# Kernel optimization log

Measured on AMD Instinct MI355X. Metric: run time of the kernel, lower is better.

Reference implementation:

```python
import jax, jax.numpy as jnp
import numpy as np

NEG = -1e30  # log-zero surrogate (avoid -inf for stable grads)


def ctc_neg_log_like(log_probs, targets, input_lengths, target_lengths):
    """Standard CTC (blank=0) negative log-likelihood, mean over batch.
    Math-equivalent to k2 topo-compile + intersect_dense + log-semiring tot_scores.
    log_probs: [B,T,C] logits or log-probs (re-normalized, as GradExpNormalize does).
    """
    lp = jax.nn.log_softmax(log_probs, axis=-1)
    B, T, C = lp.shape
    S = targets.shape[1]
    L = 2 * S + 1  # blank-interleaved extended label sequence length
    ext = jnp.zeros((B, L), jnp.int32).at[:, 1::2].set(targets.astype(jnp.int32))
    prev2 = jnp.pad(ext[:, :-2], ((0, 0), (2, 0)), constant_values=-1)
    can_skip = (ext != prev2) & (ext != 0)  # skip transition allowed

    lp_tb = jnp.moveaxis(lp, 1, 0)  # [T,B,C] for scan over time
    start = jnp.full((B, L), NEG, lp.dtype).at[:, 0].set(0.0).at[:, 1].set(0.0)
    alpha0 = start + jnp.take_along_axis(lp_tb[0], ext, axis=1)  # [B,L]

    def step(alpha, xs):
        lp_t, t = xs
        emit_t = jnp.take_along_axis(lp_t, ext, axis=1)  # [B,L]
        s1 = jnp.pad(alpha[:, :-1], ((0, 0), (1, 0)), constant_values=NEG)
        s2 = jnp.where(can_skip,
                       jnp.pad(alpha[:, :-2], ((0, 0), (2, 0)), constant_values=NEG),
                       NEG)
        new = jnp.logaddexp(jnp.logaddexp(alpha, s1), s2) + emit_t
        # freeze alpha once past this utterance's length
        new = jnp.where((t < input_lengths)[:, None], new, alpha)
        return new, None

    ts = jnp.arange(1, T, dtype=jnp.int32)
    alpha, _ = jax.lax.scan(step, alpha0, (lp_tb[1:], ts))

    idx1 = (2 * target_lengths).astype(jnp.int32)
    idx2 = jnp.maximum(2 * target_lengths - 1, 0).astype(jnp.int32)
    a1 = jnp.take_along_axis(alpha, idx1[:, None], axis=1)[:, 0]
    a2 = jnp.take_along_axis(alpha, idx2[:, None], axis=1)[:, 0]
    a2 = jnp.where(target_lengths > 0, a2, NEG)
    tot_scores = jnp.logaddexp(a1, a2)  # per-utterance log-likelihood
    return -jnp.mean(tot_scores)  # reduction='mean'


def setup_inputs() -> dict:
    key = jax.random.key(0)
    k1, k2, k3, k4 = jax.random.split(key, 4)
    B, T, C, S = 64, 2048, 1024, 256
    log_probs = jax.random.normal(k1, (B, T, C), dtype=jnp.float32)
    targets = 1 + jax.random.randint(k2, (B, S), 0, C - 1, dtype=jnp.int32)  # labels in [1, C)
    input_lengths = jax.random.randint(k3, (B,), T // 2, T + 1, dtype=jnp.int32)
    target_lengths = jax.random.randint(k4, (B,), S // 2, S + 1, dtype=jnp.int32)
    return {"log_probs": log_probs, "targets": targets,
            "input_lengths": input_lengths, "target_lengths": target_lengths}


def reference(log_probs, targets, input_lengths, target_lengths):
    return ctc_neg_log_like(log_probs, targets, input_lengths, target_lengths)
```

## Files before the change

kernel.cpp:

```cpp
#include <hip/hip_runtime.h>
#include <hip/hip_fp16.h>
#include <math.h>

typedef __attribute__((ext_vector_type(4))) float f32x4;
typedef __attribute__((ext_vector_type(2))) unsigned int u32x2;

#define SB() __builtin_amdgcn_sched_barrier(0)
#define WAITV(n)                                              \
  do {                                                        \
    asm volatile("s_waitcnt vmcnt(" #n ")" ::: "memory");     \
    SB();                                                     \
  } while (0)
#define LD2(dst, ptr, OFF)                                           \
  asm volatile("global_load_dwordx2 %0, %1, off offset:" OFF         \
               : "=v"(dst) : "v"(ptr) : "memory")
#define LD4(dst, ptr, OFF)                                           \
  asm volatile("global_load_dwordx4 %0, %1, off offset:" OFF         \
               : "=v"(dst) : "v"(ptr) : "memory")

__device__ inline float wave_max64(float v) {
#pragma unroll
  for (int off = 32; off > 0; off >>= 1) v = fmaxf(v, __shfl_xor(v, off, 64));
  return v;
}
__device__ inline float wave_sum64(float v) {
#pragma unroll
  for (int off = 32; off > 0; off >>= 1) v += __shfl_xor(v, off, 64);
  return v;
}
__device__ inline float wave_max_dpp(float x) {
  int xi = __float_as_int(x);
  x = fmaxf(x, __int_as_float(__builtin_amdgcn_update_dpp(xi, xi, 0x111, 0xf, 0xf, false)));
  xi = __float_as_int(x);
  x = fmaxf(x, __int_as_float(__builtin_amdgcn_update_dpp(xi, xi, 0x112, 0xf, 0xf, false)));
  xi = __float_as_int(x);
  x = fmaxf(x, __int_as_float(__builtin_amdgcn_update_dpp(xi, xi, 0x114, 0xf, 0xf, false)));
  xi = __float_as_int(x);
  x = fmaxf(x, __int_as_float(__builtin_amdgcn_update_dpp(xi, xi, 0x118, 0xf, 0xf, false)));
  xi = __float_as_int(x);
  x = fmaxf(x, __int_as_float(__builtin_amdgcn_update_dpp(xi, xi, 0x142, 0xa, 0xf, false)));
  xi = __float_as_int(x);
  x = fmaxf(x, __int_as_float(__builtin_amdgcn_update_dpp(xi, xi, 0x143, 0xc, 0xf, false)));
  return __int_as_float(__builtin_amdgcn_readlane(__float_as_int(x), 63));
}
__device__ inline float lane_shr1(float x) {
  return __int_as_float(__builtin_amdgcn_update_dpp(
      0, __float_as_int(x), 0x138, 0xf, 0xf, true));
}

__device__ __forceinline__ void k1_body(
    const float* __restrict__ lp, const int* __restrict__ targets,
    char* __restrict__ gw, float* __restrict__ qw, int t0, int T, int CB,
    int QS, int S, int b, int tq, float* rowbuf) {
  const int lane = threadIdx.x & 63;
  const int w = threadIdx.x >> 6;
  const int tloc = tq * 4 + w;
  const int t = t0 + tloc;
  if (t >= T) return;
  const int4 tg4 = *(const int4*)(targets + (size_t)b * S + 4 * lane);

  const float* row = lp + ((size_t)b * T + t) * 1024;
  const float4 v0 = *(const float4*)(row + 4 * lane);
  const float4 v1 = *(const float4*)(row + 256 + 4 * lane);
  const float4 v2 = *(const float4*)(row + 512 + 4 * lane);
  const float4 v3 = *(const float4*)(row + 768 + 4 * lane);
  float mx = fmaxf(fmaxf(fmaxf(v0.x, v0.y), fmaxf(v0.z, v0.w)),
                   fmaxf(fmaxf(v1.x, v1.y), fmaxf(v1.z, v1.w)));
  mx = fmaxf(mx, fmaxf(fmaxf(fmaxf(v2.x, v2.y), fmaxf(v2.z, v2.w)),
                       fmaxf(fmaxf(v3.x, v3.y), fmaxf(v3.z, v3.w))));
  mx = wave_max64(mx);
  float sm = __expf(v0.x - mx) + __expf(v0.y - mx) + __expf(v0.z - mx) +
             __expf(v0.w - mx) + __expf(v1.x - mx) + __expf(v1.y - mx) +
             __expf(v1.z - mx) + __expf(v1.w - mx) + __expf(v2.x - mx) +
             __expf(v2.y - mx) + __expf(v2.z - mx) + __expf(v2.w - mx) +
             __expf(v3.x - mx) + __expf(v3.y - mx) + __expf(v3.z - mx) +
             __expf(v3.w - mx);
  sm = wave_sum64(sm);
  const float lse = mx + __logf(sm);
  *(float4*)(rowbuf + 4 * lane) = v0;
  *(float4*)(rowbuf + 256 + 4 * lane) = v1;
  *(float4*)(rowbuf + 512 + 4 * lane) = v2;
  *(float4*)(rowbuf + 768 + 4 * lane) = v3;
  const float e0 = __expf(rowbuf[tg4.x] - lse);
  const float e1 = __expf(rowbuf[tg4.y] - lse);
  const float e2 = __expf(rowbuf[tg4.z] - lse);
  const float e3 = __expf(rowbuf[tg4.w] - lse);
  const unsigned h0 = __half_as_ushort(__float2half(e0));
  const unsigned h1 = __half_as_ushort(__float2half(e1));
  const unsigned h2 = __half_as_ushort(__float2half(e2));
  const unsigned h3 = __half_as_ushort(__float2half(e3));
  char* gr = gw + ((size_t)b * CB + tloc) * 544;
  *(uint2*)(gr + 8 * lane) = make_uint2(h0 | (h1 << 16), h2 | (h3 << 16));
  if (lane == 0) qw[(size_t)b * QS + tloc] = __expf(rowbuf[0] - lse);
}

__global__ __launch_bounds__(256) void k1_std(
    const float* __restrict__ lp, const int* __restrict__ targets,
    char* __restrict__ gw, float* __restrict__ qw, int t0, int T, int CB,
    int QS, int S) {
  __shared__ __align__(16) float rowbuf4[4][1024];
  k1_body(lp, targets, gw, qw, t0, T, CB, QS, S, blockIdx.y, blockIdx.x,
          rowbuf4[threadIdx.x >> 6]);
}

#define DECL8(P)                                                     \
  u32x2 P##v0, P##v1, P##v2, P##v3, P##v4, P##v5, P##v6, P##v7;      \
  f32x4 P##qL, P##qH;

#define ISS8(P)                                                      \
  do {                                                               \
    LD2(P##v0, gpA_, "0");    LD2(P##v1, gpA_, "544");               \
    LD2(P##v2, gpA_, "1088"); LD2(P##v3, gpA_, "1632");              \
    LD2(P##v4, gpB_, "0");    LD2(P##v5, gpB_, "544");               \
    LD2(P##v6, gpB_, "1088"); LD2(P##v7, gpB_, "1632");              \
    LD4(P##qL, gq_, "0");     LD4(P##qH, gq_, "16");                 \
    gpA_ += 4352; gpB_ += 4352; gq_ += 8;                            \
  } while (0)

#define KSR(du, qv)                                                           \
  {                                                                           \
    const float px = __half2float(__ushort_as_half((unsigned short)((du).x))); \
    const float py = __half2float(__ushort_as_half((unsigned short)((du).x >> 16))); \
    const float pz = __half2float(__ushort_as_half((unsigned short)((du).y))); \
    const float pw = __half2float(__ushort_as_half((unsigned short)((du).y >> 16))); \
    const float hm1 = lane_shr1(a7);                                          \
    const float n0 = (a0 + hm1) * (qv);                                       \
    const float n1 = __fmaf_rn(sk1, hm1, a1 + a0) * px;                       \
    const float n2 = (a2 + a1) * (qv);                                        \
    const float n3 = __fmaf_rn(sk3, a1, a3 + a2) * py;                        \
    const float n4 = (a4 + a3) * (qv);                                        \
    const float n5 = __fmaf_rn(sk5, a3, a5 + a4) * pz;                        \
    const float n6 = (a6 + a5) * (qv);                                        \
    const float n7 = __fmaf_rn(sk7, a5, a7 + a6) * pw;                        \
    const float n8 = (a8 + a7) * (qv);                                        \
    a0 = n0; a1 = n1; a2 = n2; a3 = n3; a4 = n4;                              \
    a5 = n5; a6 = n6; a7 = n7; a8 = n8;                                       \
  }

#define RESC()                                                            \
  {                                                                       \
    float m_ = fmaxf(fmaxf(fmaxf(fmaxf(a0, a1), fmaxf(a2, a3)),           \
                           fmaxf(fmaxf(a4, a5), fmaxf(a6, a7))), a8);     \
    m_ = wave_max_dpp(m_);                                                \
    const int e_ =                                                        \
        (m_ > 0.f) ? (int)((__float_as_uint(m_) >> 23) & 255u) - 127 : 0; \
    a0 = ldexpf(a0, -e_); a1 = ldexpf(a1, -e_); a2 = ldexpf(a2, -e_);     \
    a3 = ldexpf(a3, -e_); a4 = ldexpf(a4, -e_); a5 = ldexpf(a5, -e_);     \
    a6 = ldexpf(a6, -e_); a7 = ldexpf(a7, -e_); a8 = ldexpf(a8, -e_);     \
    E += e_;                                                              \
  }

#define COMP8(P, rem)                                            \
  do {                                                           \
    if ((rem) >= 8) {                                            \
      KSR(P##v0, (P##qL).x) KSR(P##v1, (P##qL).y)                \
      KSR(P##v2, (P##qL).z) KSR(P##v3, (P##qL).w)                \
      KSR(P##v4, (P##qH).x) KSR(P##v5, (P##qH).y)                \
      KSR(P##v6, (P##qH).z) KSR(P##v7, (P##qH).w) RESC()         \
    } else {                                                     \
      KSR(P##v0, (P##qL).x)                                      \
      if ((rem) > 1) KSR(P##v1, (P##qL).y)                       \
      if ((rem) > 2) KSR(P##v2, (P##qL).z)                       \
      if ((rem) > 3) KSR(P##v3, (P##qL).w)                       \
      if ((rem) > 4) KSR(P##v4, (P##qH).x)                       \
      if ((rem) > 5) KSR(P##v5, (P##qH).y)                       \
      if ((rem) > 6) KSR(P##v6, (P##qH).z)                       \
      RESC()                                                     \
    }                                                            \
  } while (0)

template <int R0, int LAST>
__device__ __forceinline__ void k2_body(
    const char* __restrict__ gb, const float* __restrict__ qb,
    const int* __restrict__ targets, const int* __restrict__ in_len,
    const int* __restrict__ tgt_len, float* __restrict__ alpha_g,
    int* __restrict__ exp_g, float* __restrict__ tot, int b, int t0, int Tc,
    int S) {
  const int lane = threadIdx.x & 63;
  const int len = in_len[b];
  const int tl = tgt_len[b];
  const int* tg = targets + (size_t)b * S;
  const int4 mytg = *(const int4*)(tg + 4 * lane);
  const int tgm1 = (lane > 0) ? tg[4 * lane - 1] : -1;
  const float sk1 = (lane > 0 && mytg.x != tgm1) ? 1.f : 0.f;
  const float sk3 = (mytg.y != mytg.x) ? 1.f : 0.f;
  const float sk5 = (mytg.z != mytg.y) ? 1.f : 0.f;
  const float sk7 = (mytg.w != mytg.z) ? 1.f : 0.f;

  float a0 = 0.f, a1 = 0.f, a2 = 0.f, a3 = 0.f, a4 = 0.f, a5 = 0.f, a6 = 0.f,
        a7 = 0.f, a8 = 0.f;
  int E = 0;
  if (R0) {
    if (lane == 0) {
      a0 = qb[0];
      a1 = __half2float(*(const __half*)gb);
    }
  } else {
    const float* ap = alpha_g + (size_t)b * 520 + 8 * lane;
    a0 = ap[0]; a1 = ap[1]; a2 = ap[2]; a3 = ap[3];
    a4 = ap[4]; a5 = ap[5]; a6 = ap[6]; a7 = ap[7];
    a8 = (lane == 63) ? alpha_g[(size_t)b * 520 + 512] : 0.f;
    E = exp_g[b];
  }

  const int t_hi = min(t0 + Tc, len);
  int N = t_hi - (t0 + R0);
  if (N < 0) N = 0;
  const int G = (N + 7) >> 3;

  const char* gpA_ = gb + (size_t)R0 * 544 + 8 * lane;
  const char* gpB_ = gpA_ + 2176;
  const float* gq_ = qb + R0;

  DECL8(A) DECL8(B)

  __builtin_amdgcn_s_setprio(1);
  asm volatile("s_waitcnt vmcnt(0) lgkmcnt(0)" ::: "memory");
  SB();
  ISS8(A); ISS8(B);

  for (int g = 0; g < G; g += 2) {
    WAITV(10);
    COMP8(A, N - 8 * g);
    ISS8(A);
    if (g + 1 < G) {
      WAITV(10);
      COMP8(B, N - 8 * (g + 1));
      ISS8(B);
    }
  }
  WAITV(0);
  __builtin_amdgcn_s_setprio(0);

  if constexpr (LAST) {
    __shared__ float fin[520];
    fin[8 * lane + 0] = a0; fin[8 * lane + 1] = a1;
    fin[8 * lane + 2] = a2; fin[8 * lane + 3] = a3;
    fin[8 * lane + 4] = a4; fin[8 * lane + 5] = a5;
    fin[8 * lane + 6] = a6; fin[8 * lane + 7] = a7;
    if (lane == 63) fin[512] = a8;
    asm volatile("s_waitcnt lgkmcnt(0)" ::: "memory");
    SB();
    if (lane == 0) {
      const int i1 = 2 * tl;
      const int i2 = (2 * tl - 1 > 0) ? (2 * tl - 1) : 0;
      float v = fin[i1] + ((tl > 0) ? fin[i2] : 0.f);
      v = fmaxf(v, 1e-37f);
      tot[b] = logf(v) + (float)E * 0.6931471805599453f;
    }
  } else {
    float* ap = alpha_g + (size_t)b * 520 + 8 * lane;
    ap[0] = a0; ap[1] = a1; ap[2] = a2; ap[3] = a3;
    ap[4] = a4; ap[5] = a5; ap[6] = a6; ap[7] = a7;
    if (lane == 63) alpha_g[(size_t)b * 520 + 512] = a8;
    if (lane == 0) exp_g[b] = E;
  }
}

template <int R0, int LAST>
__global__ __launch_bounds__(64, 1) void k2_std(
    const char* __restrict__ gbuf, const float* __restrict__ qbuf,
    const int* __restrict__ targets, const int* __restrict__ in_len,
    const int* __restrict__ tgt_len, float* __restrict__ alpha_g,
    int* __restrict__ exp_g, float* __restrict__ tot, int t0, int Tc, int CB,
    int QS, int S) {
  k2_body<R0, LAST>(gbuf + (size_t)blockIdx.x * CB * 544,
                    qbuf + (size_t)blockIdx.x * QS, targets, in_len, tgt_len,
                    alpha_g, exp_g, tot, blockIdx.x, t0, Tc, S);
}

template <int R0>
__global__ __launch_bounds__(256, 1) void fused_k(
    const float* __restrict__ lp, const int* __restrict__ targets,
    const int* __restrict__ in_len, const int* __restrict__ tgt_len,
    float* __restrict__ alpha_g, int* __restrict__ exp_g,
    float* __restrict__ tot, const char* __restrict__ gprev,
    const float* __restrict__ qprev, char* __restrict__ gcur,
    float* __restrict__ qcur, int t0k2, int t0k1, int T, int Tc, int CB,
    int QS, int S, int TQ4) {
  __shared__ __align__(16) float rowbuf4[4][1024];
  if (blockIdx.x < 64) {
    if (threadIdx.x >= 64) return;
    k2_body<R0, 0>(gprev + (size_t)blockIdx.x * CB * 544,
                   qprev + (size_t)blockIdx.x * QS, targets, in_len, tgt_len,
                   alpha_g, exp_g, tot, blockIdx.x, t0k2, Tc, S);
    return;
  }
  const int id = blockIdx.x - 64;
  const int b = id / TQ4;
  const int tq = id - b * TQ4;
  k1_body(lp, targets, gcur, qcur, t0k1, T, CB, QS, S, b, tq,
          rowbuf4[threadIdx.x >> 6]);
}

__global__ void k3_mean(const float* __restrict__ tot, float* __restrict__ out,
                        int B) {
  float v = (threadIdx.x < B) ? tot[threadIdx.x] : 0.0f;
  v = wave_sum64(v);
  if (threadIdx.x == 0) out[0] = -v / (float)B;
}

extern "C" void kernel_launch(void* const* d_in, const int* in_sizes, int n_in,
                              void* d_out, int out_size, void* d_ws,
                              size_t ws_size, hipStream_t stream) {
  const float* lp = (const float*)d_in[0];
  const int* targets = (const int*)d_in[1];
  const int* in_len = (const int*)d_in[2];
  const int* tgt_len = (const int*)d_in[3];
  float* out = (float*)d_out;

  const int B = in_sizes[2];
  const int S = in_sizes[1] / B;
  const int C = 1024;
  const int T = (int)((size_t)in_sizes[0] / ((size_t)B * C));

  const size_t headf = 64 + 64 + (size_t)64 * 520;
  int Tc = 512;
  if (Tc > T) Tc = T;
  int CB = 0, QS = 0;
  while (Tc >= 64) {
    CB = Tc + 64;
    QS = Tc + 64;
    const size_t need =
        (headf + 2 * (size_t)64 * QS) * 4 + 2 * (size_t)64 * CB * 544;
    if (need <= ws_size || Tc == 64) break;
    Tc >>= 1;
  }
  const int nch = (T + Tc - 1) / Tc;
  const int TQ4 = Tc / 4;

  float* tot = (float*)d_ws;
  int* exp_g = (int*)(tot + 64);
  float* alpha_g = (float*)(exp_g + 64);
  float* q0 = alpha_g + (size_t)64 * 520;
  float* q1 = q0 + (size_t)64 * QS;
  char* g0 = (char*)(q1 + (size_t)64 * QS);
  char* g1 = g0 + (size_t)64 * CB * 544;
  char* gbuf[2] = {g0, g1};
  float* qbuf[2] = {q0, q1};

  if (nch == 1) {
    k1_std<<<dim3(TQ4, B), 256, 0, stream>>>(lp, targets, gbuf[0], qbuf[0], 0,
                                             T, CB, QS, S);
    k2_std<1, 1><<<B, 64, 0, stream>>>(gbuf[0], qbuf[0], targets, in_len,
                                       tgt_len, alpha_g, exp_g, tot, 0, Tc,
                                       CB, QS, S);
  } else {
    k1_std<<<dim3(TQ4, B), 256, 0, stream>>>(lp, targets, gbuf[0], qbuf[0], 0,
                                             T, CB, QS, S);
    for (int c = 1; c < nch; ++c) {
      const int t0k2 = (c - 1) * Tc;
      const int t0k1 = c * Tc;
      const dim3 grid(64 + TQ4 * B);
      if (c == 1)
        fused_k<1><<<grid, 256, 0, stream>>>(
            lp, targets, in_len, tgt_len, alpha_g, exp_g, tot,
            gbuf[(c - 1) & 1], qbuf[(c - 1) & 1], gbuf[c & 1], qbuf[c & 1],
            t0k2, t0k1, T, Tc, CB, QS, S, TQ4);
      else
        fused_k<0><<<grid, 256, 0, stream>>>(
            lp, targets, in_len, tgt_len, alpha_g, exp_g, tot,
            gbuf[(c - 1) & 1], qbuf[(c - 1) & 1], gbuf[c & 1], qbuf[c & 1],
            t0k2, t0k1, T, Tc, CB, QS, S, TQ4);
    }
    const int cl = nch - 1;
    k2_std<0, 1><<<B, 64, 0, stream>>>(gbuf[cl & 1], qbuf[cl & 1], targets,
                                       in_len, tgt_len, alpha_g, exp_g, tot,
                                       cl * Tc, Tc, CB, QS, S);
  }
  k3_mean<<<1, 64, 0, stream>>>(tot, out, B);
}
```

Measured before the change: 239.6 us.

## Pack eight waves per block for log-softmax and CTC recurrence kernels

```diff
diff --git a/kernel.cpp b/kernel.cpp
--- a/kernel.cpp
+++ b/kernel.cpp
@@ -48,13 +48,13 @@
       0, __float_as_int(x), 0x138, 0xf, 0xf, true));
 }
 
-__device__ __forceinline__ void k1_body(
+__device__ __forceinline__ void k1_body8(
     const float* __restrict__ lp, const int* __restrict__ targets,
     char* __restrict__ gw, float* __restrict__ qw, int t0, int T, int CB,
     int QS, int S, int b, int tq, float* rowbuf) {
   const int lane = threadIdx.x & 63;
   const int w = threadIdx.x >> 6;
-  const int tloc = tq * 4 + w;
+  const int tloc = tq * 8 + w;
   const int t = t0 + tloc;
   if (t >= T) return;
   const int4 tg4 = *(const int4*)(targets + (size_t)b * S + 4 * lane);
@@ -94,13 +94,13 @@
   if (lane == 0) qw[(size_t)b * QS + tloc] = __expf(rowbuf[0] - lse);
 }
 
-__global__ __launch_bounds__(256) void k1_std(
+__global__ __launch_bounds__(512) void k1_std8(
     const float* __restrict__ lp, const int* __restrict__ targets,
     char* __restrict__ gw, float* __restrict__ qw, int t0, int T, int CB,
     int QS, int S) {
-  __shared__ __align__(16) float rowbuf4[4][1024];
-  k1_body(lp, targets, gw, qw, t0, T, CB, QS, S, blockIdx.y, blockIdx.x,
-          rowbuf4[threadIdx.x >> 6]);
+  __shared__ __align__(16) float lds[8192];
+  k1_body8(lp, targets, gw, qw, t0, T, CB, QS, S, blockIdx.y, blockIdx.x,
+           lds + (threadIdx.x >> 6) * 1024);
 }
 
 #define DECL8(P)                                                     \
@@ -175,7 +175,7 @@
     const int* __restrict__ targets, const int* __restrict__ in_len,
     const int* __restrict__ tgt_len, float* __restrict__ alpha_g,
     int* __restrict__ exp_g, float* __restrict__ tot, int b, int t0, int Tc,
-    int S) {
+    int S, float* fin) {
   const int lane = threadIdx.x & 63;
   const int len = in_len[b];
   const int tl = tgt_len[b];
@@ -233,7 +233,6 @@
   __builtin_amdgcn_s_setprio(0);
 
   if constexpr (LAST) {
-    __shared__ float fin[520];
     fin[8 * lane + 0] = a0; fin[8 * lane + 1] = a1;
     fin[8 * lane + 2] = a2; fin[8 * lane + 3] = a3;
     fin[8 * lane + 4] = a4; fin[8 * lane + 5] = a5;
@@ -258,39 +257,43 @@
 }
 
 template <int R0, int LAST>
-__global__ __launch_bounds__(64, 1) void k2_std(
+__global__ __launch_bounds__(512) void k2_std8(
     const char* __restrict__ gbuf, const float* __restrict__ qbuf,
     const int* __restrict__ targets, const int* __restrict__ in_len,
     const int* __restrict__ tgt_len, float* __restrict__ alpha_g,
     int* __restrict__ exp_g, float* __restrict__ tot, int t0, int Tc, int CB,
     int QS, int S) {
-  k2_body<R0, LAST>(gbuf + (size_t)blockIdx.x * CB * 544,
-                    qbuf + (size_t)blockIdx.x * QS, targets, in_len, tgt_len,
-                    alpha_g, exp_g, tot, blockIdx.x, t0, Tc, S);
+  __shared__ float fin[8][520];
+  const int w = threadIdx.x >> 6;
+  const int b = blockIdx.x * 8 + w;
+  k2_body<R0, LAST>(gbuf + (size_t)b * CB * 544, qbuf + (size_t)b * QS,
+                    targets, in_len, tgt_len, alpha_g, exp_g, tot, b, t0, Tc,
+                    S, fin[w]);
 }
 
 template <int R0>
-__global__ __launch_bounds__(256, 1) void fused_k(
+__global__ __launch_bounds__(512) void fused8(
     const float* __restrict__ lp, const int* __restrict__ targets,
     const int* __restrict__ in_len, const int* __restrict__ tgt_len,
     float* __restrict__ alpha_g, int* __restrict__ exp_g,
     float* __restrict__ tot, const char* __restrict__ gprev,
     const float* __restrict__ qprev, char* __restrict__ gcur,
     float* __restrict__ qcur, int t0k2, int t0k1, int T, int Tc, int CB,
-    int QS, int S, int TQ4) {
-  __shared__ __align__(16) float rowbuf4[4][1024];
-  if (blockIdx.x < 64) {
-    if (threadIdx.x >= 64) return;
-    k2_body<R0, 0>(gprev + (size_t)blockIdx.x * CB * 544,
-                   qprev + (size_t)blockIdx.x * QS, targets, in_len, tgt_len,
-                   alpha_g, exp_g, tot, blockIdx.x, t0k2, Tc, S);
+    int QS, int S, int TQ8) {
+  __shared__ __align__(16) float lds[8192];
+  const int w = threadIdx.x >> 6;
+  if (blockIdx.x < 8) {
+    const int b = blockIdx.x * 8 + w;
+    k2_body<R0, 0>(gprev + (size_t)b * CB * 544, qprev + (size_t)b * QS,
+                   targets, in_len, tgt_len, alpha_g, exp_g, tot, b, t0k2, Tc,
+                   S, nullptr);
     return;
   }
-  const int id = blockIdx.x - 64;
-  const int b = id / TQ4;
-  const int tq = id - b * TQ4;
-  k1_body(lp, targets, gcur, qcur, t0k1, T, CB, QS, S, b, tq,
-          rowbuf4[threadIdx.x >> 6]);
+  const int id = blockIdx.x - 8;
+  const int b = id / TQ8;
+  const int tq = id - b * TQ8;
+  k1_body8(lp, targets, gcur, qcur, t0k1, T, CB, QS, S, b, tq,
+           lds + w * 1024);
 }
 
 __global__ void k3_mean(const float* __restrict__ tot, float* __restrict__ out,
@@ -327,7 +330,7 @@
     Tc >>= 1;
   }
   const int nch = (T + Tc - 1) / Tc;
-  const int TQ4 = Tc / 4;
+  const int TQ8 = Tc / 8;
 
   float* tot = (float*)d_ws;
   int* exp_g = (int*)(tot + 64);
@@ -340,33 +343,33 @@
   float* qbuf[2] = {q0, q1};
 
   if (nch == 1) {
-    k1_std<<<dim3(TQ4, B), 256, 0, stream>>>(lp, targets, gbuf[0], qbuf[0], 0,
-                                             T, CB, QS, S);
-    k2_std<1, 1><<<B, 64, 0, stream>>>(gbuf[0], qbuf[0], targets, in_len,
-                                       tgt_len, alpha_g, exp_g, tot, 0, Tc,
-                                       CB, QS, S);
+    k1_std8<<<dim3(TQ8, B), 512, 0, stream>>>(lp, targets, gbuf[0], qbuf[0],
+                                              0, T, CB, QS, S);
+    k2_std8<1, 1><<<8, 512, 0, stream>>>(gbuf[0], qbuf[0], targets, in_len,
+                                         tgt_len, alpha_g, exp_g, tot, 0, Tc,
+                                         CB, QS, S);
   } else {
-    k1_std<<<dim3(TQ4, B), 256, 0, stream>>>(lp, targets, gbuf[0], qbuf[0], 0,
-                                             T, CB, QS, S);
+    k1_std8<<<dim3(TQ8, B), 512, 0, stream>>>(lp, targets, gbuf[0], qbuf[0],
+                                              0, T, CB, QS, S);
     for (int c = 1; c < nch; ++c) {
       const int t0k2 = (c - 1) * Tc;
       const int t0k1 = c * Tc;
-      const dim3 grid(64 + TQ4 * B);
+      const dim3 grid(8 + TQ8 * B);
       if (c == 1)
-        fused_k<1><<<grid, 256, 0, stream>>>(
+        fused8<1><<<grid, 512, 0, stream>>>(
             lp, targets, in_len, tgt_len, alpha_g, exp_g, tot,
             gbuf[(c - 1) & 1], qbuf[(c - 1) & 1], gbuf[c & 1], qbuf[c & 1],
-            t0k2, t0k1, T, Tc, CB, QS, S, TQ4);
+            t0k2, t0k1, T, Tc, CB, QS, S, TQ8);
       else
-        fused_k<0><<<grid, 256, 0, stream>>>(
+        fused8<0><<<grid, 512, 0, stream>>>(
             lp, targets, in_len, tgt_len, alpha_g, exp_g, tot,
             gbuf[(c - 1) & 1], qbuf[(c - 1) & 1], gbuf[c & 1], qbuf[c & 1],
-            t0k2, t0k1, T, Tc, CB, QS, S, TQ4);
+            t0k2, t0k1, T, Tc, CB, QS, S, TQ8);
     }
     const int cl = nch - 1;
-    k2_std<0, 1><<<B, 64, 0, stream>>>(gbuf[cl & 1], qbuf[cl & 1], targets,
-                                       in_len, tgt_len, alpha_g, exp_g, tot,
-                                       cl * Tc, Tc, CB, QS, S);
+    k2_std8<0, 1><<<8, 512, 0, stream>>>(gbuf[cl & 1], qbuf[cl & 1], targets,
+                                         in_len, tgt_len, alpha_g, exp_g, tot,
+                                         cl * Tc, Tc, CB, QS, S);
   }
   k3_mean<<<1, 64, 0, stream>>>(tot, out, B);
 }
```

New measurement: 344.4 us. 43.7% more time.
